# Kernel optimization log

Hardware: AMD Instinct MI355X
Metric: run time of the kernel (lower is better)

The kernel has to match this reference:

```python
import jax, jax.numpy as jnp
import numpy as np

H = 8
NEG = -1e9


def setup_inputs() -> dict:
    key = jax.random.key(0)
    ks = jax.random.split(key, 16)
    B, S, D = 4, 512, 512
    dk = D // H
    NUM_REL = 20 * 2 + 1  # 41
    s_in = 1.0 / np.sqrt(D)
    s_emb = np.sqrt(6.0 / (NUM_REL + dk))  # xavier_uniform
    inp = {
        "query": jax.random.normal(ks[0], (B, S, D), jnp.float32),
        "key": jax.random.normal(ks[1], (B, S, D), jnp.float32),
        "value": jax.random.normal(ks[2], (B, S, D), jnp.float32),
        "mask": jax.random.randint(ks[3], (B, S, S), 0, NUM_REL, jnp.int32),
        # linear layers stored as [in, out] (y = x @ W + b)
        "Wq": jax.random.normal(ks[4], (D, D), jnp.float32) * s_in,
        "bq": jnp.zeros((D,), jnp.float32),
        "Wk": jax.random.normal(ks[5], (D, D), jnp.float32) * s_in,
        "bk": jnp.zeros((D,), jnp.float32),
        "Wv": jax.random.normal(ks[6], (D, D), jnp.float32) * s_in,
        "bv": jnp.zeros((D,), jnp.float32),
        "Wo": jax.random.normal(ks[7], (D, D), jnp.float32) * s_in,
        "bo": jnp.zeros((D,), jnp.float32),
        "emb_k": jax.random.uniform(ks[8], (NUM_REL, dk), jnp.float32, -s_emb, s_emb),
        "emb_v": jax.random.uniform(ks[9], (NUM_REL, dk), jnp.float32, -s_emb, s_emb),
    }
    return inp


def reference(query, key, value, mask, Wq, bq, Wk, bk, Wv, bv, Wo, bo, emb_k, emb_v):
    B, Q, D = query.shape
    K = key.shape[1]
    dk = D // H
    # project and split heads -> [B, H, S, dk]
    q = (query @ Wq + bq).reshape(B, Q, H, dk).transpose(0, 2, 1, 3)
    k = (key @ Wk + bk).reshape(B, K, H, dk).transpose(0, 2, 1, 3)
    v = (value @ Wv + bv).reshape(B, K, H, dk).transpose(0, 2, 1, 3)
    # gather relative-position embeddings: [B, Q, K, dk]
    relem = emb_k[mask]
    relemv = emb_v[mask]
    scale = 1.0 / jnp.sqrt(jnp.asarray(dk, q.dtype))
    # content scores + relative-position bias scores
    scores = (jnp.einsum("bhqd,bhkd->bhqk", q, k)
              + jnp.einsum("bhqd,bqkd->bhqk", q, relem)) * scale
    # rmask = (mask > 0), broadcast over heads
    scores = jnp.where((mask > 0)[:, None, :, :], scores, NEG)
    attn = jax.nn.softmax(scores, axis=-1)
    # content values + relative-position value bias
    x = (jnp.einsum("bhqk,bhkd->bhqd", attn, v)
         + jnp.einsum("bhqk,bqkd->bhqd", attn, relemv))
    x = x.transpose(0, 2, 1, 3).reshape(B, Q, D)
    return x @ Wo + bo
```

## Files before the change

kernel.cpp:

```cpp
#include <hip/hip_runtime.h>

#define B_ 4
#define S_ 512
#define D_ 512
#define H_ 8
#define DK_ 64
#define NREL 41

typedef __attribute__((ext_vector_type(8))) short bf16x8;
typedef __attribute__((ext_vector_type(4))) float f32x4;

__device__ __forceinline__ unsigned short f2bf(float f) {
  unsigned u = __float_as_uint(f);
  u = u + 0x7FFFu + ((u >> 16) & 1u);
  return (unsigned short)(u >> 16);
}

#define MFMA16(a, b, c) __builtin_amdgcn_mfma_f32_16x16x32_bf16((a), (b), (c), 0, 0, 0)

#define LDS_FENCE() do { \
  asm volatile("s_waitcnt lgkmcnt(0)" ::: "memory"); \
  __builtin_amdgcn_sched_barrier(0); \
} while (0)

struct PrepArgs { const float* W[4]; const float* in[3]; };

__global__ __launch_bounds__(256) void prep(PrepArgs PA,
    const float* __restrict__ embk, const float* __restrict__ embv,
    const int* __restrict__ mask,
    ushort* __restrict__ WT0, ushort* __restrict__ ekb, ushort* __restrict__ evt,
    ushort* __restrict__ inbf0, uchar* __restrict__ mask8)
{
  const int z = blockIdx.z;
  const int t = threadIdx.x;
  if (z == 4) {
    int lb = blockIdx.y * 8 + blockIdx.x;
    size_t base = (size_t)lb * 16384;
    #pragma unroll
    for (int i = 0; i < 16; ++i) {
      size_t off = base + (size_t)i * 1024 + t * 4;
      int4 v = *(const int4*)&mask[off];
      uchar4 pk;
      pk.x = (uchar)v.x; pk.y = (uchar)v.y; pk.z = (uchar)v.z; pk.w = (uchar)v.w;
      *(uchar4*)&mask8[off] = pk;
    }
    if (lb == 0) {
      for (int i = t; i < 48 * 64; i += 256) {
        int r = i >> 6, d = i & 63;
        ekb[i] = (r < NREL) ? f2bf(embk[r * 64 + d]) : (ushort)0;
      }
      for (int i = t; i < 64 * 64; i += 256) {
        int d = i >> 6, r = i & 63;
        evt[i] = (r < NREL) ? f2bf(embv[r * 64 + d]) : (ushort)0;
      }
    }
    return;
  }
  if (z >= 5) {
    const float* src = PA.in[z - 5];
    ushort* dst = inbf0 + (size_t)(z - 5) * ((size_t)2048 * 512);
    int lb = blockIdx.y * 8 + blockIdx.x;
    size_t base = (size_t)lb * 16384;
    #pragma unroll
    for (int i = 0; i < 16; ++i) {
      size_t off = base + (size_t)i * 1024 + t * 4;
      float4 v = *(const float4*)&src[off];
      ushort4 pk;
      pk.x = f2bf(v.x); pk.y = f2bf(v.y); pk.z = f2bf(v.z); pk.w = f2bf(v.w);
      *(ushort4*)&dst[off] = pk;
    }
    return;
  }
  __shared__ float sh[64][65];
  const float* W = PA.W[z];
  ushort* WT = WT0 + (size_t)z * (D_ * D_);
  const int k0 = blockIdx.x * 64, n0 = blockIdx.y * 64;
  const int rr = t >> 4, cc = (t & 15) * 4;
  #pragma unroll
  for (int i = 0; i < 4; ++i) {
    float4 v = *(const float4*)&W[(size_t)(k0 + rr + i * 16) * D_ + n0 + cc];
    sh[rr + i * 16][cc + 0] = v.x; sh[rr + i * 16][cc + 1] = v.y;
    sh[rr + i * 16][cc + 2] = v.z; sh[rr + i * 16][cc + 3] = v.w;
  }
  __syncthreads();
  #pragma unroll
  for (int i = 0; i < 4; ++i) {
    int r2 = rr + i * 16;
    ushort4 pk;
    pk.x = f2bf(sh[cc + 0][r2]); pk.y = f2bf(sh[cc + 1][r2]);
    pk.z = f2bf(sh[cc + 2][r2]); pk.w = f2bf(sh[cc + 3][r2]);
    *(ushort4*)&WT[(size_t)(n0 + r2) * D_ + k0 + cc] = pk;
  }
}

struct GemmP  { const ushort* A; const ushort* Wt; const float* bias; void* out;
                int mode; int kbeg; int kend; float oscale; };
struct GemmPs { GemmP p[3]; };

__global__ __launch_bounds__(256) void gemm_bf16(GemmPs P)
{
  __shared__ ushort As[64][72];
  __shared__ ushort Bs[64][72];
  const GemmP gp = P.p[blockIdx.z];
  const int t = threadIdx.x, l = t & 63, w = t >> 6;
  const int r16 = l & 15, g4 = l >> 4;
  const int wmo = (w >> 1) * 32, wno = (w & 1) * 32;
  const int m0 = blockIdx.x * 64, n0 = blockIdx.y * 64;

  f32x4 acc[2][2];
  #pragma unroll
  for (int mi = 0; mi < 2; ++mi)
    #pragma unroll
    for (int ni = 0; ni < 2; ++ni) acc[mi][ni] = 0.0f;

  const int srow = t >> 2, sseg = (t & 3) * 16;
  for (int k0 = gp.kbeg; k0 < gp.kend; k0 += 64) {
    __syncthreads();
    *(uint4*)&As[srow][sseg]     = *(const uint4*)&gp.A[(size_t)(m0 + srow) * D_ + k0 + sseg];
    *(uint4*)&As[srow][sseg + 8] = *(const uint4*)&gp.A[(size_t)(m0 + srow) * D_ + k0 + sseg + 8];
    *(uint4*)&Bs[srow][sseg]     = *(const uint4*)&gp.Wt[(size_t)(n0 + srow) * D_ + k0 + sseg];
    *(uint4*)&Bs[srow][sseg + 8] = *(const uint4*)&gp.Wt[(size_t)(n0 + srow) * D_ + k0 + sseg + 8];
    __syncthreads();
    #pragma unroll
    for (int kk = 0; kk < 2; ++kk) {
      bf16x8 af[2], bfr[2];
      #pragma unroll
      for (int i = 0; i < 2; ++i) af[i]  = *(const bf16x8*)&As[wmo + i * 16 + r16][kk * 32 + g4 * 8];
      #pragma unroll
      for (int i = 0; i < 2; ++i) bfr[i] = *(const bf16x8*)&Bs[wno + i * 16 + r16][kk * 32 + g4 * 8];
      #pragma unroll
      for (int mi = 0; mi < 2; ++mi)
        #pragma unroll
        for (int ni = 0; ni < 2; ++ni)
          acc[mi][ni] = MFMA16(af[mi], bfr[ni], acc[mi][ni]);
    }
  }

  #pragma unroll
  for (int mi = 0; mi < 2; ++mi) {
    #pragma unroll
    for (int ni = 0; ni < 2; ++ni) {
      int n = n0 + wno + ni * 16 + r16;
      int mb = m0 + wmo + mi * 16 + g4 * 4;
      if (gp.mode == 3) {
        float* PO = (float*)gp.out;
        #pragma unroll
        for (int r = 0; r < 4; ++r) PO[(size_t)(mb + r) * D_ + n] = acc[mi][ni][r];
      } else {
        float bv = gp.bias[n];
        ushort* O = (ushort*)gp.out;
        int h = n >> 6, d = n & 63;
        if (gp.mode == 1) {
          #pragma unroll
          for (int r = 0; r < 4; ++r) {
            int m = mb + r, b = m >> 9, s = m & 511;
            O[(((size_t)(b * H_ + h)) * S_ + s) * DK_ + d] = f2bf((acc[mi][ni][r] + bv) * gp.oscale);
          }
        } else {
          int b = mb >> 9, s = mb & 511;
          ushort4 pk;
          pk.x = f2bf(acc[mi][ni][0] + bv); pk.y = f2bf(acc[mi][ni][1] + bv);
          pk.z = f2bf(acc[mi][ni][2] + bv); pk.w = f2bf(acc[mi][ni][3] + bv);
          *(ushort4*)&O[(((size_t)(b * H_ + h)) * DK_ + d) * S_ + s] = pk;
        }
      }
    }
  }
}

__global__ __launch_bounds__(256, 2) void attn_mfma(
    const ushort* __restrict__ qb,
    const ushort* __restrict__ kb,
    const ushort* __restrict__ vtb,
    const uchar* __restrict__ mask8,
    const ushort* __restrict__ ekb,
    const ushort* __restrict__ evt,
    float* __restrict__ part,
    float* __restrict__ sums)
{
  __shared__ float  qrelS[4][16][48];
  __shared__ float  wrS[4][16][44];
  __shared__ ushort PbS[4][16][72];
  const int t = threadIdx.x, w = t >> 6, l = t & 63;
  const int g = blockIdx.x;
  const int h = g & 7, b = (g >> 3) & 3, chunk = (g >> 5) & 1, qtg = g >> 6;
  const int qt = qtg * 4 + w;
  const int bh = b * H_ + h;
  const int r16 = l & 15, g4 = l >> 4;
  float  (*qrel)[48] = qrelS[w];
  float  (*wr)[44]   = wrS[w];
  ushort (*Pb)[72]   = PbS[w];

  {
    float* wrf = &wr[0][0];
    #pragma unroll
    for (int i = 0; i < 11; ++i) wrf[i * 64 + l] = 0.f;
  }

  const size_t qoff = ((size_t)bh * S_ + qt * 16) * DK_;
  bf16x8 qf0 = *(const bf16x8*)&qb[qoff + (size_t)r16 * DK_ + g4 * 8];
  bf16x8 qf1 = *(const bf16x8*)&qb[qoff + (size_t)r16 * DK_ + 32 + g4 * 8];

  {
    #pragma unroll
    for (int s = 0; s < 3; ++s) {
      bf16x8 e0 = *(const bf16x8*)&ekb[(s * 16 + r16) * 64 + g4 * 8];
      bf16x8 e1 = *(const bf16x8*)&ekb[(s * 16 + r16) * 64 + 32 + g4 * 8];
      f32x4 qr = 0.0f;
      qr = MFMA16(qf0, e0, qr);
      qr = MFMA16(qf1, e1, qr);
      #pragma unroll
      for (int r = 0; r < 4; ++r) qrel[g4 * 4 + r][s * 16 + r16] = qr[r];
    }
  }
  LDS_FENCE();

  float ssum[4] = {0.f, 0.f, 0.f, 0.f};
  f32x4 oacc[4];
  #pragma unroll
  for (int i = 0; i < 4; ++i) oacc[i] = 0.0f;

  const uchar* mbase = mask8 + ((size_t)b * S_ + qt * 16) * S_;
  const size_t voff = (size_t)bh * DK_ * S_;
  const int kt0 = chunk * 4;

  #pragma unroll 1
  for (int kti = 0; kti < 4; ++kti) {
    const int kt = kt0 + kti;
    const size_t koff = ((size_t)bh * S_ + kt * 64) * DK_;
    bf16x8 kf0[4], kf1[4];
    #pragma unroll
    for (int sub = 0; sub < 4; ++sub) {
      kf0[sub] = *(const bf16x8*)&kb[koff + (size_t)(sub * 16 + r16) * DK_ + g4 * 8];
      kf1[sub] = *(const bf16x8*)&kb[koff + (size_t)(sub * 16 + r16) * DK_ + 32 + g4 * 8];
    }
    f32x4 sacc[4];
    #pragma unroll
    for (int sub = 0; sub < 4; ++sub) {
      f32x4 z = 0.0f;
      z = MFMA16(qf0, kf0[sub], z);
      z = MFMA16(qf1, kf1[sub], z);
      sacc[sub] = z;
    }
    bf16x8 vf0[4], vf1[4];
    #pragma unroll
    for (int ds = 0; ds < 4; ++ds) {
      vf0[ds] = *(const bf16x8*)&vtb[voff + (size_t)(ds * 16 + r16) * S_ + kt * 64 + g4 * 8];
      vf1[ds] = *(const bf16x8*)&vtb[voff + (size_t)(ds * 16 + r16) * S_ + kt * 64 + 32 + g4 * 8];
    }
    int mv[16];
    #pragma unroll
    for (int sub = 0; sub < 4; ++sub)
      #pragma unroll
      for (int r = 0; r < 4; ++r)
        mv[sub * 4 + r] = mbase[(size_t)(g4 * 4 + r) * S_ + kt * 64 + sub * 16 + r16];
    float qv[16];
    #pragma unroll
    for (int i = 0; i < 16; ++i) qv[i] = qrel[g4 * 4 + (i & 3)][mv[i]];
    #pragma unroll
    for (int sub = 0; sub < 4; ++sub) {
      #pragma unroll
      for (int r = 0; r < 4; ++r) {
        int i = sub * 4 + r;
        float e = (mv[i] > 0) ? __expf(sacc[sub][r] + qv[i]) : 0.f;
        ssum[r] += e;
        atomicAdd(&wr[g4 * 4 + r][mv[i]], e);
        Pb[g4 * 4 + r][sub * 16 + r16] = f2bf(e);
      }
    }
    LDS_FENCE();
    bf16x8 pf0 = *(const bf16x8*)&Pb[r16][g4 * 8];
    bf16x8 pf1 = *(const bf16x8*)&Pb[r16][32 + g4 * 8];
    LDS_FENCE();
    #pragma unroll
    for (int ds = 0; ds < 4; ++ds) {
      oacc[ds] = MFMA16(pf0, vf0[ds], oacc[ds]);
      oacc[ds] = MFMA16(pf1, vf1[ds], oacc[ds]);
    }
  }

  #pragma unroll
  for (int i = 0; i < 16; ++i) {
    int col = g4 * 16 + i;
    Pb[r16][col] = (col < 44) ? f2bf(wr[r16][col]) : (ushort)0;
  }
  LDS_FENCE();
  {
    bf16x8 wf0 = *(const bf16x8*)&Pb[r16][g4 * 8];
    bf16x8 wf1 = *(const bf16x8*)&Pb[r16][32 + g4 * 8];
    #pragma unroll
    for (int ds = 0; ds < 4; ++ds) {
      bf16x8 e0 = *(const bf16x8*)&evt[(ds * 16 + r16) * 64 + g4 * 8];
      bf16x8 e1 = *(const bf16x8*)&evt[(ds * 16 + r16) * 64 + 32 + g4 * 8];
      oacc[ds] = MFMA16(wf0, e0, oacc[ds]);
      oacc[ds] = MFMA16(wf1, e1, oacc[ds]);
    }
  }

  #pragma unroll
  for (int m = 1; m < 16; m <<= 1)
    #pragma unroll
    for (int r = 0; r < 4; ++r) ssum[r] += __shfl_xor(ssum[r], m);

  #pragma unroll
  for (int r = 0; r < 4; ++r) {
    int q = qt * 16 + g4 * 4 + r;
    float* dst = part + (((size_t)chunk * B_ + b) * S_ + q) * D_ + h * DK_;
    #pragma unroll
    for (int ds = 0; ds < 4; ++ds) dst[ds * 16 + r16] = oacc[ds][r];
  }
  if (r16 == 0) {
    size_t sb = ((size_t)chunk * 32 + bh) * S_ + qt * 16 + g4 * 4;
    sums[sb + 0] = ssum[0]; sums[sb + 1] = ssum[1];
    sums[sb + 2] = ssum[2]; sums[sb + 3] = ssum[3];
  }
}

__global__ __launch_bounds__(256) void attn_reduce(
    const float* __restrict__ part, const float* __restrict__ sums,
    ushort* __restrict__ ctx)
{
  int idx = blockIdx.x * 256 + threadIdx.x;
  int d4 = idx & 127;
  int s  = (idx >> 7) & 511;
  int b  = idx >> 16;
  int h  = d4 >> 4;
  float sm = 0.f;
  #pragma unroll
  for (int c = 0; c < 2; ++c) sm += sums[((size_t)c * 32 + b * 8 + h) * S_ + s];
  float inv = 1.f / sm;
  float4 o = make_float4(0.f, 0.f, 0.f, 0.f);
  #pragma unroll
  for (int c = 0; c < 2; ++c) {
    float4 p = *(const float4*)&part[(((size_t)c * B_ + b) * S_ + s) * D_ + d4 * 4];
    o.x += p.x; o.y += p.y; o.z += p.z; o.w += p.w;
  }
  ushort4 pk;
  pk.x = f2bf(o.x * inv); pk.y = f2bf(o.y * inv);
  pk.z = f2bf(o.z * inv); pk.w = f2bf(o.w * inv);
  *(ushort4*)&ctx[((size_t)b * S_ + s) * D_ + d4 * 4] = pk;
}

__global__ __launch_bounds__(256) void out_reduce(
    const float* __restrict__ po, const float* __restrict__ bo,
    float* __restrict__ out)
{
  int idx = blockIdx.x * 256 + threadIdx.x;
  int n4 = (idx & 127) * 4;
  size_t off = (size_t)idx * 4;
  float4 a = *(const float4*)&po[off];
  float4 c = *(const float4*)&po[off + (size_t)2048 * 512];
  float4 bb = *(const float4*)&bo[n4];
  float4 o = make_float4(a.x + c.x + bb.x, a.y + c.y + bb.y,
                         a.z + c.z + bb.z, a.w + c.w + bb.w);
  *(float4*)&out[off] = o;
}

extern "C" void kernel_launch(void* const* d_in, const int* in_sizes, int n_in,
                              void* d_out, int out_size, void* d_ws, size_t ws_size,
                              hipStream_t stream) {
  (void)in_sizes; (void)n_in; (void)out_size; (void)ws_size;
  const float* query = (const float*)d_in[0];
  const float* key   = (const float*)d_in[1];
  const float* value = (const float*)d_in[2];
  const int*   mask  = (const int*)d_in[3];
  const float* Wq = (const float*)d_in[4];
  const float* bq = (const float*)d_in[5];
  const float* Wk = (const float*)d_in[6];
  const float* bk = (const float*)d_in[7];
  const float* Wv = (const float*)d_in[8];
  const float* bv = (const float*)d_in[9];
  const float* Wo = (const float*)d_in[10];
  const float* bo = (const float*)d_in[11];
  const float* embk = (const float*)d_in[12];
  const float* embv = (const float*)d_in[13];
  float* out = (float*)d_out;

  const size_t MD  = (size_t)2048 * 512;
  const size_t WSZ = (size_t)D_ * D_;
  ushort* wsu  = (ushort*)d_ws;
  ushort* WT   = wsu;
  ushort* ekb  = WT + 4 * WSZ;
  ushort* evt  = ekb + 3072;
  ushort* qbf  = evt + 4096;
  ushort* kbf  = qbf + MD;
  ushort* vtbf = kbf + MD;
  ushort* ctx  = vtbf + MD;
  ushort* inbf = ctx + MD;
  float*  sums = (float*)(inbf + 3 * MD);
  float*  part = sums + (size_t)4 * 32 * 512;
  float*  po   = part;
  uchar*  mask8 = (uchar*)(part + 4 * MD);

  PrepArgs PA;
  PA.W[0] = Wq; PA.W[1] = Wk; PA.W[2] = Wv; PA.W[3] = Wo;
  PA.in[0] = query; PA.in[1] = key; PA.in[2] = value;
  prep<<<dim3(8, 8, 8), 256, 0, stream>>>(PA, embk, embv, mask, WT, ekb, evt, inbf, mask8);

  GemmPs P1;
  P1.p[0] = { inbf,          WT + 0 * WSZ, bq, qbf,  1, 0, 512, 0.125f };
  P1.p[1] = { inbf + MD,     WT + 1 * WSZ, bk, kbf,  1, 0, 512, 1.0f };
  P1.p[2] = { inbf + 2 * MD, WT + 2 * WSZ, bv, vtbf, 2, 0, 512, 1.0f };
  gemm_bf16<<<dim3(32, 8, 3), 256, 0, stream>>>(P1);

  attn_mfma<<<dim3(512), 256, 0, stream>>>(qbf, kbf, vtbf, mask8, ekb, evt, part, sums);
  attn_reduce<<<dim3(1024), 256, 0, stream>>>(part, sums, ctx);

  GemmPs P2;
  P2.p[0] = { ctx, WT + 3 * WSZ, nullptr, po,      3, 0,   256, 1.0f };
  P2.p[1] = { ctx, WT + 3 * WSZ, nullptr, po + MD, 3, 256, 512, 1.0f };
  P2.p[2] = P2.p[0];
  gemm_bf16<<<dim3(32, 8, 2), 256, 0, stream>>>(P2);

  out_reduce<<<dim3(1024), 256, 0, stream>>>(po, bo, out);
}
```

Baseline: 172.7 us.

## Stage K/V tiles and mask in swizzled shared memory with register-prefetch double buffering

Each of the four waves previously loaded the same K and V tiles and its own mask rows straight from global memory. Now the block loads each K/V tile once into XOR-swizzled LDS double buffers, prefetching the next tile into registers during compute, and stages the block's mask slab in LDS up front. This removes redundant global traffic across waves and overlaps loads with MFMA work. In exchange it uses much more LDS (about 48KB), adds block-wide barriers every iteration, and drops the 2-blocks-per-SIMD launch bound, which may reduce occupancy.

```diff
diff --git a/kernel.cpp b/kernel.cpp
--- a/kernel.cpp
+++ b/kernel.cpp
@@ -168,7 +168,7 @@
   }
 }
 
-__global__ __launch_bounds__(256, 2) void attn_mfma(
+__global__ __launch_bounds__(256) void attn_mfma(
     const ushort* __restrict__ qb,
     const ushort* __restrict__ kb,
     const ushort* __restrict__ vtb,
@@ -178,6 +178,9 @@
     float* __restrict__ part,
     float* __restrict__ sums)
 {
+  __shared__ ushort Kbuf[2][4096];
+  __shared__ ushort Vbuf[2][4096];
+  __shared__ uchar  maskT[64 * 256];
   __shared__ float  qrelS[4][16][48];
   __shared__ float  wrS[4][16][44];
   __shared__ ushort PbS[4][16][72];
@@ -190,6 +193,25 @@
   float  (*qrel)[48] = qrelS[w];
   float  (*wr)[44]   = wrS[w];
   ushort (*Pb)[72]   = PbS[w];
+  const int kt0 = chunk * 4;
+  const int u0 = t, u1 = t + 256;
+  const int kr0 = u0 >> 3, kc0 = u0 & 7, kr1 = u1 >> 3, kc1 = u1 & 7;
+  const int ks0 = (kc0 ^ (kr0 & 7)) * 8, ks1 = (kc1 ^ (kr1 & 7)) * 8;
+
+  const uchar* msrc = mask8 + ((size_t)(b * S_ + qtg * 64)) * S_ + chunk * 256;
+  uint4 mreg[4];
+  #pragma unroll
+  for (int i = 0; i < 4; ++i) {
+    int unit = t + i * 256;
+    mreg[i] = *(const uint4*)&msrc[(size_t)(unit >> 4) * S_ + (unit & 15) * 16];
+  }
+  const ushort* ksrc = kb + ((size_t)bh * S_ + kt0 * 64) * DK_;
+  const ushort* vsrc = vtb + (size_t)bh * DK_ * S_ + kt0 * 64;
+  uint4 kreg0 = *(const uint4*)&ksrc[kr0 * 64 + kc0 * 8];
+  uint4 kreg1 = *(const uint4*)&ksrc[kr1 * 64 + kc1 * 8];
+  uint4 vreg0 = *(const uint4*)&vsrc[(size_t)kr0 * S_ + kc0 * 8];
+  uint4 vreg1 = *(const uint4*)&vsrc[(size_t)kr1 * S_ + kc1 * 8];
+  __builtin_amdgcn_sched_barrier(0);
 
   {
     float* wrf = &wr[0][0];
@@ -213,47 +235,52 @@
       for (int r = 0; r < 4; ++r) qrel[g4 * 4 + r][s * 16 + r16] = qr[r];
     }
   }
-  LDS_FENCE();
+
+  #pragma unroll
+  for (int i = 0; i < 4; ++i) {
+    int unit = t + i * 256;
+    *(uint4*)&maskT[unit * 16] = mreg[i];
+  }
+  *(uint4*)&Kbuf[0][kr0 * 64 + ks0] = kreg0;
+  *(uint4*)&Kbuf[0][kr1 * 64 + ks1] = kreg1;
+  *(uint4*)&Vbuf[0][kr0 * 64 + ks0] = vreg0;
+  *(uint4*)&Vbuf[0][kr1 * 64 + ks1] = vreg1;
+  __syncthreads();
 
   float ssum[4] = {0.f, 0.f, 0.f, 0.f};
   f32x4 oacc[4];
   #pragma unroll
   for (int i = 0; i < 4; ++i) oacc[i] = 0.0f;
 
-  const uchar* mbase = mask8 + ((size_t)b * S_ + qt * 16) * S_;
-  const size_t voff = (size_t)bh * DK_ * S_;
-  const int kt0 = chunk * 4;
-
-  #pragma unroll 1
+  #pragma unroll
   for (int kti = 0; kti < 4; ++kti) {
-    const int kt = kt0 + kti;
-    const size_t koff = ((size_t)bh * S_ + kt * 64) * DK_;
-    bf16x8 kf0[4], kf1[4];
+    const int cur = kti & 1;
+    if (kti < 3) {
+      const ushort* kn = kb + ((size_t)bh * S_ + (kt0 + kti + 1) * 64) * DK_;
+      const ushort* vn = vtb + (size_t)bh * DK_ * S_ + (kt0 + kti + 1) * 64;
+      kreg0 = *(const uint4*)&kn[kr0 * 64 + kc0 * 8];
+      kreg1 = *(const uint4*)&kn[kr1 * 64 + kc1 * 8];
+      vreg0 = *(const uint4*)&vn[(size_t)kr0 * S_ + kc0 * 8];
+      vreg1 = *(const uint4*)&vn[(size_t)kr1 * S_ + kc1 * 8];
+      __builtin_amdgcn_sched_barrier(0);
+    }
+    f32x4 sacc[4];
     #pragma unroll
     for (int sub = 0; sub < 4; ++sub) {
-      kf0[sub] = *(const bf16x8*)&kb[koff + (size_t)(sub * 16 + r16) * DK_ + g4 * 8];
-      kf1[sub] = *(const bf16x8*)&kb[koff + (size_t)(sub * 16 + r16) * DK_ + 32 + g4 * 8];
-    }
-    f32x4 sacc[4];
-    #pragma unroll
-    for (int sub = 0; sub < 4; ++sub) {
+      int krow = sub * 16 + r16;
+      bf16x8 kf0 = *(const bf16x8*)&Kbuf[cur][krow * 64 + ((g4 ^ (krow & 7)) * 8)];
+      bf16x8 kf1 = *(const bf16x8*)&Kbuf[cur][krow * 64 + (((g4 + 4) ^ (krow & 7)) * 8)];
       f32x4 z = 0.0f;
-      z = MFMA16(qf0, kf0[sub], z);
-      z = MFMA16(qf1, kf1[sub], z);
+      z = MFMA16(qf0, kf0, z);
+      z = MFMA16(qf1, kf1, z);
       sacc[sub] = z;
     }
-    bf16x8 vf0[4], vf1[4];
-    #pragma unroll
-    for (int ds = 0; ds < 4; ++ds) {
-      vf0[ds] = *(const bf16x8*)&vtb[voff + (size_t)(ds * 16 + r16) * S_ + kt * 64 + g4 * 8];
-      vf1[ds] = *(const bf16x8*)&vtb[voff + (size_t)(ds * 16 + r16) * S_ + kt * 64 + 32 + g4 * 8];
-    }
     int mv[16];
     #pragma unroll
     for (int sub = 0; sub < 4; ++sub)
       #pragma unroll
       for (int r = 0; r < 4; ++r)
-        mv[sub * 4 + r] = mbase[(size_t)(g4 * 4 + r) * S_ + kt * 64 + sub * 16 + r16];
+        mv[sub * 4 + r] = maskT[(w * 16 + g4 * 4 + r) * 256 + kti * 64 + sub * 16 + r16];
     float qv[16];
     #pragma unroll
     for (int i = 0; i < 16; ++i) qv[i] = qrel[g4 * 4 + (i & 3)][mv[i]];
@@ -274,9 +301,19 @@
     LDS_FENCE();
     #pragma unroll
     for (int ds = 0; ds < 4; ++ds) {
-      oacc[ds] = MFMA16(pf0, vf0[ds], oacc[ds]);
-      oacc[ds] = MFMA16(pf1, vf1[ds], oacc[ds]);
-    }
+      int vrow = ds * 16 + r16;
+      bf16x8 vf0 = *(const bf16x8*)&Vbuf[cur][vrow * 64 + ((g4 ^ (vrow & 7)) * 8)];
+      bf16x8 vf1 = *(const bf16x8*)&Vbuf[cur][vrow * 64 + (((g4 + 4) ^ (vrow & 7)) * 8)];
+      oacc[ds] = MFMA16(pf0, vf0, oacc[ds]);
+      oacc[ds] = MFMA16(pf1, vf1, oacc[ds]);
+    }
+    if (kti < 3) {
+      *(uint4*)&Kbuf[cur ^ 1][kr0 * 64 + ks0] = kreg0;
+      *(uint4*)&Kbuf[cur ^ 1][kr1 * 64 + ks1] = kreg1;
+      *(uint4*)&Vbuf[cur ^ 1][kr0 * 64 + ks0] = vreg0;
+      *(uint4*)&Vbuf[cur ^ 1][kr1 * 64 + ks1] = vreg1;
+    }
+    __syncthreads();
   }
 
   #pragma unroll
```

After: 174.1 us. About the same (+0.8%).
